# Kernel tuning notes

Measured on AMD Instinct MI355X. Metric: run time of the kernel, lower is better.

Reference implementation:

```python
import jax, jax.numpy as jnp
import numpy as np


def fwht(x):
    """Normalized fast Walsh-Hadamard transform along last dim (== matmul_hadU).
    x[..., n] with n a power of 2; returns H_n @ x / sqrt(n) (Sylvester ordering).
    """
    orig_shape = x.shape
    n = orig_shape[-1]
    x = x.reshape(-1, n)
    h = 1
    while h < n:
        # pair elements at distance h: butterfly (a+b, a-b)
        x = x.reshape(-1, n // (2 * h), 2, h)
        a = x[:, :, 0:1, :]
        b = x[:, :, 1:2, :]
        x = jnp.concatenate([a + b, a - b], axis=2).reshape(-1, n)
        h *= 2
    scale = jnp.asarray(1.0 / np.sqrt(n), x.dtype)
    return (x * scale).reshape(orig_shape)


def setup_inputs() -> dict:
    key = jax.random.key(0)
    k1, k2, k3 = jax.random.split(key, 3)
    B, S, D_IN, D_OUT = 4, 2048, 4096, 4096
    x = jax.random.normal(k1, (B, S, D_IN), dtype=jnp.float32)
    W = jax.random.normal(k2, (D_OUT, D_IN), dtype=jnp.float32) * (1.0 / np.sqrt(D_IN))
    b = jax.random.normal(k3, (D_OUT,), dtype=jnp.float32)
    return {"x": x, "W": W, "b": b}


def reference(x, W, b):
    # Hadamard rotation of the activations, then Linear: y = fwht(x) @ W.T + b
    rotated = fwht(x)                                   # [B, S, D_in]
    return jnp.einsum("bsd,od->bso", rotated, W) + b    # [B, S, D_out]
```

## Files before the change

### kernel.cpp

```cpp
#include <hip/hip_runtime.h>
#include <hip/hip_bf16.h>
#include <cstdint>
#include <cstddef>

typedef __bf16 bf16_t;
typedef bf16_t bf16x8 __attribute__((ext_vector_type(8)));
typedef float  f32x4  __attribute__((ext_vector_type(4)));

#define FWHT_N 4096

#define BM 256
#define BN 256
#define KSTEP 32
#define ABYTES 16384
#define BUFBYTES 32768
#define NBUF 4

__device__ __forceinline__ void fwht16(float v[16]) {
#pragma unroll
    for (int h = 1; h < 16; h <<= 1) {
#pragma unroll
        for (int i = 0; i < 16; ++i) {
            if (!(i & h)) {
                const float a = v[i];
                const float b = v[i | h];
                v[i]     = a + b;
                v[i | h] = a - b;
            }
        }
    }
}

__device__ __forceinline__ int pad(int i) { return i + (i >> 5); }

__global__ __launch_bounds__(256) void fwht_rows_bf16(const float* __restrict__ W,
                                                      bf16_t* __restrict__ Wt) {
    __shared__ float lds[FWHT_N + (FWHT_N >> 5)];
    const int r = blockIdx.x;
    const int t = threadIdx.x;

    float v[16];

    const float4* src = (const float4*)(W + (size_t)r * FWHT_N + 16 * t);
    {
        const float4 a0 = src[0], a1 = src[1], a2 = src[2], a3 = src[3];
        v[0] = a0.x; v[1] = a0.y; v[2]  = a0.z; v[3]  = a0.w;
        v[4] = a1.x; v[5] = a1.y; v[6]  = a1.z; v[7]  = a1.w;
        v[8] = a2.x; v[9] = a2.y; v[10] = a2.z; v[11] = a2.w;
        v[12] = a3.x; v[13] = a3.y; v[14] = a3.z; v[15] = a3.w;
    }
    fwht16(v);
    {
        const int base = 16 * t + (t >> 1);
#pragma unroll
        for (int k = 0; k < 16; ++k) lds[base + k] = v[k];
    }
    __syncthreads();

    const int b1 = ((t >> 4) << 8) | (t & 15);
#pragma unroll
    for (int k = 0; k < 16; ++k) v[k] = lds[pad(b1 + (k << 4))];
    fwht16(v);
#pragma unroll
    for (int k = 0; k < 16; ++k) lds[pad(b1 + (k << 4))] = v[k];
    __syncthreads();

#pragma unroll
    for (int k = 0; k < 16; ++k) v[k] = lds[pad(t + (k << 8))];
    fwht16(v);

    const float s = 0.015625f;
    bf16_t* dst = Wt + (size_t)r * FWHT_N + t;
#pragma unroll
    for (int k = 0; k < 16; ++k) dst[k << 8] = (bf16_t)(v[k] * s);
}

__global__ __launch_bounds__(256) void cvt_f32_bf16(const float4* __restrict__ x,
                                                    bf16x8* __restrict__ y) {
    const size_t i = (size_t)blockIdx.x * 256 + threadIdx.x;
    const float4 a = x[2 * i];
    const float4 b = x[2 * i + 1];
    bf16x8 o;
    o[0] = (bf16_t)a.x; o[1] = (bf16_t)a.y; o[2] = (bf16_t)a.z; o[3] = (bf16_t)a.w;
    o[4] = (bf16_t)b.x; o[5] = (bf16_t)b.y; o[6] = (bf16_t)b.z; o[7] = (bf16_t)b.w;
    y[i] = o;
}

__device__ __forceinline__ void g2lds16(const bf16_t* g, bf16_t* l) {
    __builtin_amdgcn_global_load_lds((__attribute__((address_space(1))) void*)g,
                                     (__attribute__((address_space(3))) void*)l,
                                     16, 0, 0);
}

__global__ __launch_bounds__(512, 2) void gemm256_bt_bias(
    const bf16_t* __restrict__ A,
    const bf16_t* __restrict__ Bm,
    const float* __restrict__ bias,
    float* __restrict__ C,
    int M, int N, int K)
{
    __shared__ __align__(16) char lds[NBUF * BUFBYTES];

    const int tid  = threadIdx.x;
    const int wave = tid >> 6;
    const int lane = tid & 63;
    const int quad = lane >> 4;
    const int l16  = lane & 15;

    const int nbx  = N / BN;
    const int flat = blockIdx.y * nbx + blockIdx.x;
    const int per  = (nbx * (M / BM)) >> 3;
    const int nf   = (flat & 7) * per + (flat >> 3);
    const int m0   = (nf / nbx) * BM;
    const int n0   = (nf % nbx) * BN;

    const int wm = (wave >> 2) * 128;
    const int wn = (wave & 3) * 64;

    const int srow = wave * 16 + (lane >> 2);
    const int scb  = (((lane & 3) ^ ((lane >> 3) & 3)) << 4);
    const int L0   = wave * 1024 + lane * 16;

    const bf16_t* gA0 = A  + (size_t)(m0 + srow)       * K + (scb >> 1);
    const bf16_t* gA1 = A  + (size_t)(m0 + srow + 128) * K + (scb >> 1);
    const bf16_t* gB0 = Bm + (size_t)(n0 + srow)       * K + (scb >> 1);
    const bf16_t* gB1 = Bm + (size_t)(n0 + srow + 128) * K + (scb >> 1);

    const int cbr   = ((quad ^ ((lane >> 1) & 3)) << 4);
    const int aoff  = l16 * 64 + cbr;
    const int abase = ((wm >> 4) << 10) + aoff;
    const int bbase = ABYTES + ((wn >> 4) << 10) + aoff;

    f32x4 acc[8][4] = {};
    bf16x8 aF0[8], bF0[4], aF1[8], bF1[4];

    const int NT = K / KSTEP;

    auto stageTo = [&](int s) {
        char* d = &lds[(s & (NBUF - 1)) * BUFBYTES];
        const int ko = (s < NT ? s : NT - 1) * KSTEP;
        g2lds16(gA0 + ko, (bf16_t*)(d + L0));
        g2lds16(gA1 + ko, (bf16_t*)(d + L0 + 8192));
        g2lds16(gB0 + ko, (bf16_t*)(d + ABYTES + L0));
        g2lds16(gB1 + ko, (bf16_t*)(d + ABYTES + L0 + 8192));
    };
    auto loadFrags = [&](int s, bf16x8 (&fa)[8], bf16x8 (&fb)[4]) {
        const int sc = (s < NT ? s : NT - 1);
        const char* buf = &lds[(sc & (NBUF - 1)) * BUFBYTES];
#pragma unroll
        for (int ni = 0; ni < 4; ++ni)
            fb[ni] = *(const bf16x8*)(buf + bbase + (ni << 10));
#pragma unroll
        for (int mi = 0; mi < 8; ++mi)
            fa[mi] = *(const bf16x8*)(buf + abase + (mi << 10));
    };
    auto mfmaAll = [&](bf16x8 (&fa)[8], bf16x8 (&fb)[4]) {
        __builtin_amdgcn_s_setprio(1);
#pragma unroll
        for (int mi = 0; mi < 8; ++mi)
#pragma unroll
            for (int ni = 0; ni < 4; ++ni)
                acc[mi][ni] = __builtin_amdgcn_mfma_f32_16x16x32_bf16(
                    fa[mi], fb[ni], acc[mi][ni], 0, 0, 0);
        __builtin_amdgcn_s_setprio(0);
    };

    stageTo(0);
    stageTo(1);
    asm volatile("s_waitcnt vmcnt(4)" ::: "memory");
    __builtin_amdgcn_s_barrier();
    __builtin_amdgcn_sched_barrier(0);
    loadFrags(0, aF0, bF0);
    stageTo(2);

#pragma unroll 1
    for (int s = 0; s < NT; s += 2) {
        asm volatile("s_waitcnt vmcnt(4)" ::: "memory");
        __builtin_amdgcn_s_barrier();
        __builtin_amdgcn_sched_barrier(0);
        loadFrags(s + 1, aF1, bF1);
        stageTo(s + 3);
        mfmaAll(aF0, bF0);

        asm volatile("s_waitcnt vmcnt(4)" ::: "memory");
        __builtin_amdgcn_s_barrier();
        __builtin_amdgcn_sched_barrier(0);
        loadFrags(s + 2, aF0, bF0);
        stageTo(s + 4);
        mfmaAll(aF1, bF1);
    }
    asm volatile("s_waitcnt vmcnt(0)" ::: "memory");

    const int crow = quad * 4;
#pragma unroll
    for (int ni = 0; ni < 4; ++ni) {
        const int n  = n0 + wn + ni * 16 + l16;
        const float bv = bias[n];
#pragma unroll
        for (int mi = 0; mi < 8; ++mi) {
            const int mb = m0 + wm + mi * 16 + crow;
#pragma unroll
            for (int r = 0; r < 4; ++r)
                C[(size_t)(mb + r) * N + n] = acc[mi][ni][r] + bv;
        }
    }
}

extern "C" void kernel_launch(void* const* d_in, const int* in_sizes, int n_in,
                              void* d_out, int out_size, void* d_ws, size_t ws_size,
                              hipStream_t stream) {
    const float* x = (const float*)d_in[0];
    const float* W = (const float*)d_in[1];
    const float* b = (const float*)d_in[2];
    float* out = (float*)d_out;

    const int K = 4096;
    const int N = 4096;
    const int M = in_sizes[0] / K;

    bf16_t* xb = (bf16_t*)d_ws;
    bf16_t* Wt = xb + (size_t)M * K;

    hipLaunchKernelGGL(fwht_rows_bf16, dim3(N), dim3(256), 0, stream, W, Wt);

    const int cvt_blocks = (int)(((size_t)M * K) / 8 / 256);
    hipLaunchKernelGGL(cvt_f32_bf16, dim3(cvt_blocks), dim3(256), 0, stream,
                       (const float4*)x, (bf16x8*)xb);

    hipLaunchKernelGGL(gemm256_bt_bias, dim3(N / BN, M / BM), dim3(512), 0, stream,
                       xb, Wt, b, out, M, N, K);
}
```

Baseline: 492.1 us.

## Restructure GEMM main loop into four half-tile phases with split staging

Replaces the two-stage double-buffered fragment pipeline with a four-phase schedule per iteration. Each phase loads half the A fragments, issues half of the global-to-LDS staging, synchronizes, then runs 16 MFMAs, with vmcnt waits at half boundaries. This cuts live fragment registers and interleaves LDS reads, global loads and MFMAs more finely, but adds more barriers per K step, which may stall waves.

```diff
diff --git a/kernel.cpp b/kernel.cpp
--- a/kernel.cpp
+++ b/kernel.cpp
@@ -132,64 +132,94 @@
     const int bbase = ABYTES + ((wn >> 4) << 10) + aoff;
 
     f32x4 acc[8][4] = {};
-    bf16x8 aF0[8], bF0[4], aF1[8], bF1[4];
+    bf16x8 aF[4], aG[4], bE[4], bO[4];
 
     const int NT = K / KSTEP;
-
-    auto stageTo = [&](int s) {
+    const int NIT = NT / 2;
+
+    auto stageHalf = [&](int s, int h) {
         char* d = &lds[(s & (NBUF - 1)) * BUFBYTES];
         const int ko = (s < NT ? s : NT - 1) * KSTEP;
-        g2lds16(gA0 + ko, (bf16_t*)(d + L0));
-        g2lds16(gA1 + ko, (bf16_t*)(d + L0 + 8192));
-        g2lds16(gB0 + ko, (bf16_t*)(d + ABYTES + L0));
-        g2lds16(gB1 + ko, (bf16_t*)(d + ABYTES + L0 + 8192));
-    };
-    auto loadFrags = [&](int s, bf16x8 (&fa)[8], bf16x8 (&fb)[4]) {
-        const int sc = (s < NT ? s : NT - 1);
-        const char* buf = &lds[(sc & (NBUF - 1)) * BUFBYTES];
+        if (h == 0) {
+            g2lds16(gA0 + ko, (bf16_t*)(d + L0));
+            g2lds16(gA1 + ko, (bf16_t*)(d + L0 + 8192));
+        } else {
+            g2lds16(gB0 + ko, (bf16_t*)(d + ABYTES + L0));
+            g2lds16(gB1 + ko, (bf16_t*)(d + ABYTES + L0 + 8192));
+        }
+    };
+    auto dsA = [&](const char* buf, int mh, bf16x8 (&fa)[4]) {
+#pragma unroll
+        for (int i = 0; i < 4; ++i)
+            fa[i] = *(const bf16x8*)(buf + abase + ((mh * 4 + i) << 10));
+    };
+    auto dsB = [&](const char* buf, bf16x8 (&fb)[4]) {
 #pragma unroll
         for (int ni = 0; ni < 4; ++ni)
             fb[ni] = *(const bf16x8*)(buf + bbase + (ni << 10));
-#pragma unroll
-        for (int mi = 0; mi < 8; ++mi)
-            fa[mi] = *(const bf16x8*)(buf + abase + (mi << 10));
-    };
-    auto mfmaAll = [&](bf16x8 (&fa)[8], bf16x8 (&fb)[4]) {
+    };
+    auto mf16 = [&](int mh, bf16x8 (&fa)[4], bf16x8 (&fb)[4]) {
         __builtin_amdgcn_s_setprio(1);
 #pragma unroll
-        for (int mi = 0; mi < 8; ++mi)
+        for (int mi = 0; mi < 4; ++mi)
 #pragma unroll
             for (int ni = 0; ni < 4; ++ni)
-                acc[mi][ni] = __builtin_amdgcn_mfma_f32_16x16x32_bf16(
-                    fa[mi], fb[ni], acc[mi][ni], 0, 0, 0);
+                acc[mh * 4 + mi][ni] = __builtin_amdgcn_mfma_f32_16x16x32_bf16(
+                    fa[mi], fb[ni], acc[mh * 4 + mi][ni], 0, 0, 0);
         __builtin_amdgcn_s_setprio(0);
     };
 
-    stageTo(0);
-    stageTo(1);
-    asm volatile("s_waitcnt vmcnt(4)" ::: "memory");
-    __builtin_amdgcn_s_barrier();
-    __builtin_amdgcn_sched_barrier(0);
-    loadFrags(0, aF0, bF0);
-    stageTo(2);
+#define PHASE_BAR()  do { __builtin_amdgcn_s_barrier(); \
+                          asm volatile("s_waitcnt lgkmcnt(0)" ::: "memory"); \
+                          __builtin_amdgcn_sched_barrier(0); } while (0)
+#define TAIL_BAR()   do { __builtin_amdgcn_s_barrier(); \
+                          __builtin_amdgcn_sched_barrier(0); } while (0)
+#define TAIL_BARV()  do { asm volatile("s_waitcnt vmcnt(8)" ::: "memory"); \
+                          __builtin_amdgcn_s_barrier(); \
+                          __builtin_amdgcn_sched_barrier(0); } while (0)
+
+    stageHalf(0, 0); stageHalf(0, 1);
+    stageHalf(1, 0); stageHalf(1, 1);
+    stageHalf(2, 0); stageHalf(2, 1);
+    TAIL_BARV();
 
 #pragma unroll 1
-    for (int s = 0; s < NT; s += 2) {
-        asm volatile("s_waitcnt vmcnt(4)" ::: "memory");
-        __builtin_amdgcn_s_barrier();
-        __builtin_amdgcn_sched_barrier(0);
-        loadFrags(s + 1, aF1, bF1);
-        stageTo(s + 3);
-        mfmaAll(aF0, bF0);
-
-        asm volatile("s_waitcnt vmcnt(4)" ::: "memory");
-        __builtin_amdgcn_s_barrier();
-        __builtin_amdgcn_sched_barrier(0);
-        loadFrags(s + 2, aF0, bF0);
-        stageTo(s + 4);
-        mfmaAll(aF1, bF1);
+    for (int s = 0; s < NIT; ++s) {
+        const int e = 2 * s;
+        const char* bufE = &lds[(e & (NBUF - 1)) * BUFBYTES];
+        const char* bufO = &lds[((e + 1) & (NBUF - 1)) * BUFBYTES];
+
+        dsB(bufE, bE);
+        dsA(bufE, 0, aF);
+        stageHalf(e + 3, 0);
+        PHASE_BAR();
+        mf16(0, aF, bE);
+        TAIL_BAR();
+
+        dsA(bufE, 1, aG);
+        stageHalf(e + 3, 1);
+        PHASE_BAR();
+        mf16(1, aG, bE);
+        TAIL_BARV();
+
+        dsB(bufO, bO);
+        dsA(bufO, 0, aF);
+        stageHalf(e + 4, 0);
+        PHASE_BAR();
+        mf16(0, aF, bO);
+        TAIL_BAR();
+
+        dsA(bufO, 1, aG);
+        stageHalf(e + 4, 1);
+        PHASE_BAR();
+        mf16(1, aG, bO);
+        TAIL_BARV();
     }
     asm volatile("s_waitcnt vmcnt(0)" ::: "memory");
+
+#undef PHASE_BAR
+#undef TAIL_BAR
+#undef TAIL_BARV
 
     const int crow = quad * 4;
 #pragma unroll
```

New measurement: 496.3 us. No clear change (+0.9%).

## Restructure GEMM main loop to a five-buffer ring with one barrier per two k-steps

Applied to the files above, without the earlier changes.

The LDS ring grows from four to five k-step buffers. Each loop iteration now issues global-to-LDS loads for two future k-steps, then interleaves fragment loads and MFMAs across two steps, and ends with a single barrier. This halves the number of workgroup barriers and waitcnt stalls in the K loop. In exchange it uses the full 160KB of LDS and shortens the lead time between some fragment loads and their MFMAs, which can expose LDS latency.

```diff
diff --git a/kernel.cpp b/kernel.cpp
--- a/kernel.cpp
+++ b/kernel.cpp
@@ -14,7 +14,7 @@
 #define KSTEP 32
 #define ABYTES 16384
 #define BUFBYTES 32768
-#define NBUF 4
+#define NBUF 5
 
 __device__ __forceinline__ void fwht16(float v[16]) {
 #pragma unroll
@@ -132,21 +132,21 @@
     const int bbase = ABYTES + ((wn >> 4) << 10) + aoff;
 
     f32x4 acc[8][4] = {};
-    bf16x8 aF0[8], bF0[4], aF1[8], bF1[4];
+    bf16x8 aA[8], bA[4], aB[8], bB[4];
 
     const int NT = K / KSTEP;
-
-    auto stageTo = [&](int s) {
-        char* d = &lds[(s & (NBUF - 1)) * BUFBYTES];
+    const int NW = NT / 2;
+
+    auto stageStep = [&](int s, int idx) {
+        char* d = &lds[idx * BUFBYTES];
         const int ko = (s < NT ? s : NT - 1) * KSTEP;
         g2lds16(gA0 + ko, (bf16_t*)(d + L0));
         g2lds16(gA1 + ko, (bf16_t*)(d + L0 + 8192));
         g2lds16(gB0 + ko, (bf16_t*)(d + ABYTES + L0));
         g2lds16(gB1 + ko, (bf16_t*)(d + ABYTES + L0 + 8192));
     };
-    auto loadFrags = [&](int s, bf16x8 (&fa)[8], bf16x8 (&fb)[4]) {
-        const int sc = (s < NT ? s : NT - 1);
-        const char* buf = &lds[(sc & (NBUF - 1)) * BUFBYTES];
+    auto loadFrags = [&](int idx, bf16x8 (&fa)[8], bf16x8 (&fb)[4]) {
+        const char* buf = &lds[idx * BUFBYTES];
 #pragma unroll
         for (int ni = 0; ni < 4; ++ni)
             fb[ni] = *(const bf16x8*)(buf + bbase + (ni << 10));
@@ -165,30 +165,36 @@
         __builtin_amdgcn_s_setprio(0);
     };
 
-    stageTo(0);
-    stageTo(1);
+    stageStep(0, 0);
+    stageStep(1, 1);
+    stageStep(2, 2);
     asm volatile("s_waitcnt vmcnt(4)" ::: "memory");
     __builtin_amdgcn_s_barrier();
     __builtin_amdgcn_sched_barrier(0);
-    loadFrags(0, aF0, bF0);
-    stageTo(2);
-
+
+    int ib = 0;
 #pragma unroll 1
-    for (int s = 0; s < NT; s += 2) {
+    for (int w = 0; w < NW; ++w) {
+        const int e  = 2 * w;
+        const int i0 = ib;
+        const int i1 = (i0 + 1 >= NBUF) ? i0 + 1 - NBUF : i0 + 1;
+        const int i3 = (i0 + 3 >= NBUF) ? i0 + 3 - NBUF : i0 + 3;
+        const int i4 = (i0 + 4 >= NBUF) ? i0 + 4 - NBUF : i0 + 4;
+        ib = (i0 + 2 >= NBUF) ? i0 + 2 - NBUF : i0 + 2;
+
+        stageStep(e + 3, i3);
+        stageStep(e + 4, i4);
+        loadFrags(i0, aA, bA);
+        if (w) mfmaAll(aB, bB);
+        loadFrags(i1, aB, bB);
+        mfmaAll(aA, bA);
+
+        asm volatile("s_waitcnt lgkmcnt(0)" ::: "memory");
         asm volatile("s_waitcnt vmcnt(4)" ::: "memory");
         __builtin_amdgcn_s_barrier();
         __builtin_amdgcn_sched_barrier(0);
-        loadFrags(s + 1, aF1, bF1);
-        stageTo(s + 3);
-        mfmaAll(aF0, bF0);
-
-        asm volatile("s_waitcnt vmcnt(4)" ::: "memory");
-        __builtin_amdgcn_s_barrier();
-        __builtin_amdgcn_sched_barrier(0);
-        loadFrags(s + 2, aF0, bF0);
-        stageTo(s + 4);
-        mfmaAll(aF1, bF1);
-    }
+    }
+    mfmaAll(aB, bB);
     asm volatile("s_waitcnt vmcnt(0)" ::: "memory");
 
     const int crow = quad * 4;
```

Measured after the change: 491.4 us. Within noise of the previous version (-0.1%).
